# Performance work log

Hardware: AMD Instinct MI355X
Metric: run time of the kernel (lower is better)

The kernel has to match this reference:

```python
import jax, jax.numpy as jnp
import numpy as np

N_NODES = 100000
N_EDGES = 3200000
N_FEAT = 128
EMBED = 20
N_CLASSES = 10
N_GRAPHS = 64


def setup_inputs() -> dict:
    key = jax.random.key(0)
    ks = jax.random.split(key, 8)
    x = jax.random.normal(ks[0], (N_NODES, N_FEAT), dtype=jnp.float32)
    edge_index = jax.random.randint(ks[1], (2, N_EDGES), 0, N_NODES, dtype=jnp.int64)
    edge_weights = jax.random.uniform(ks[2], (N_EDGES,), dtype=jnp.float32)
    batch = jnp.sort(jax.random.randint(ks[3], (N_NODES,), 0, N_GRAPHS, dtype=jnp.int64))
    # GCNConv parameters (glorot-ish scale) and final linear layer
    W = jax.random.normal(ks[4], (N_FEAT, EMBED), dtype=jnp.float32) * (1.0 / np.sqrt(N_FEAT))
    b = jnp.zeros((EMBED,), dtype=jnp.float32)
    lin_W = jax.random.normal(ks[5], (2 * EMBED, N_CLASSES), dtype=jnp.float32) * (1.0 / np.sqrt(2 * EMBED))
    lin_b = jnp.zeros((N_CLASSES,), dtype=jnp.float32)
    return {"x": x, "edge_index": edge_index, "edge_weights": edge_weights,
            "batch": batch, "W": W, "b": b, "lin_W": lin_W, "lin_b": lin_b}


def reference(x, edge_index, edge_weights, batch, W, b, lin_W, lin_b):
    N = x.shape[0]
    # --- GCNConv with self-loops and symmetric normalization (PyG semantics) ---
    loops = jnp.arange(N, dtype=edge_index.dtype)
    src = jnp.concatenate([edge_index[0], loops])
    dst = jnp.concatenate([edge_index[1], loops])
    w = jnp.concatenate([edge_weights, jnp.ones((N,), dtype=edge_weights.dtype)])
    deg = jax.ops.segment_sum(w, dst, num_segments=N)  # degree at targets
    dinv = jnp.where(deg > 0, jax.lax.rsqrt(deg), 0.0)
    norm = dinv[src] * w * dinv[dst]  # [E+N]
    xw = x @ W  # [N, EMBED]
    msg = xw[src] * norm[:, None]  # gather + scale
    out1 = jax.ops.segment_sum(msg, dst, num_segments=N) + b  # scatter-add
    # --- L2 normalize per node (F.normalize p=2 dim=1, eps=1e-12), then ReLU ---
    nrm = jnp.sqrt(jnp.sum(out1 * out1, axis=1, keepdims=True))
    embed = jax.nn.relu(out1 / jnp.maximum(nrm, 1e-12))
    # --- global max / mean pool per graph ---
    mx = jax.ops.segment_max(embed, batch, num_segments=N_GRAPHS)
    mx = jnp.where(jnp.isfinite(mx), mx, 0.0)  # empty graphs -> 0
    cnt = jax.ops.segment_sum(jnp.ones((N,), dtype=embed.dtype), batch, num_segments=N_GRAPHS)
    mean = jax.ops.segment_sum(embed, batch, num_segments=N_GRAPHS) / jnp.maximum(cnt, 1.0)[:, None]
    pooled = jnp.concatenate([mx, mean], axis=-1)  # [G, 2*EMBED]
    return pooled @ lin_W + lin_b
```

## Files before the change

kernel.cpp:

```cpp
#include <hip/hip_runtime.h>
#include <hip/hip_fp16.h>

#define NN 100000
#define NE 3200000
#define NF 128
#define EM 20
#define NC 10
#define NG 64

#define NB 782
#define CAPB 4608
#define T 4096
#define SBLK 1024
#define NXW 391
#define GSPAN 16

__global__ __launch_bounds__(SBLK) void k_scatfat(
        const int* __restrict__ src, const int* __restrict__ dst,
        const float* __restrict__ w, int* __restrict__ gcursor,
        uint2* __restrict__ barr,
        const float* __restrict__ x, const float* __restrict__ W,
        float* __restrict__ xwf) {
    __shared__ __align__(16) char smem[52352];
    int tid = threadIdx.x;

    if (blockIdx.x < NXW) {
        float* Ws = (float*)smem;
        for (int i = tid; i < NF * EM; i += SBLK) Ws[i] = W[i];
        __syncthreads();
        int node = blockIdx.x * 256 + (tid >> 2);
        int j0 = (tid & 3) * 5;
        if (node >= NN) return;
        float acc[5] = {0.f, 0.f, 0.f, 0.f, 0.f};
        const float4* xr = (const float4*)(x + (size_t)node * NF);
        for (int k4 = 0; k4 < NF / 4; ++k4) {
            float4 xc = xr[k4];
            const float* wr = Ws + (k4 * 4) * EM + j0;
#pragma unroll
            for (int jj = 0; jj < 5; ++jj) acc[jj] = fmaf(xc.x, wr[jj], acc[jj]);
            wr += EM;
#pragma unroll
            for (int jj = 0; jj < 5; ++jj) acc[jj] = fmaf(xc.y, wr[jj], acc[jj]);
            wr += EM;
#pragma unroll
            for (int jj = 0; jj < 5; ++jj) acc[jj] = fmaf(xc.z, wr[jj], acc[jj]);
            wr += EM;
#pragma unroll
            for (int jj = 0; jj < 5; ++jj) acc[jj] = fmaf(xc.w, wr[jj], acc[jj]);
        }
        float* o = xwf + (size_t)node * EM + j0;
#pragma unroll
        for (int jj = 0; jj < 5; ++jj) o[jj] = acc[jj];
        return;
    }

    unsigned int* cnt   = (unsigned int*)smem;
    unsigned int* off   = (unsigned int*)(smem + 4096);
    unsigned int* gbase = (unsigned int*)(smem + 8192);
    unsigned int* wsum  = (unsigned int*)(smem + 11320);
    uint2*        staged= (uint2*)(smem + 11384);
    unsigned short* bkt = (unsigned short*)(smem + 44152);

    long E0 = (long)(blockIdx.x - NXW) * T;
    int tot = (int)min((long)T, (long)NE - E0);
    cnt[tid] = 0;
    __syncthreads();
    unsigned int dreg[T / SBLK];
#pragma unroll
    for (int k = 0; k < T / SBLK; ++k) {
        int e = k * SBLK + tid;
        dreg[k] = 0;
        if (e < tot) {
            dreg[k] = (unsigned)dst[E0 + e];
            atomicAdd(&cnt[dreg[k] >> 7], 1u);
        }
    }
    __syncthreads();
    {
        int lane = tid & 63, wv = tid >> 6;
        unsigned int v = cnt[tid];
        unsigned int s = v;
#pragma unroll
        for (int o = 1; o < 64; o <<= 1) {
            unsigned int t = __shfl_up(s, o);
            if (lane >= o) s += t;
        }
        if (lane == 63) wsum[wv] = s;
        __syncthreads();
        if (tid == 0) {
            unsigned int a = 0;
#pragma unroll
            for (int i = 0; i < 16; ++i) { unsigned int t = wsum[i]; wsum[i] = a; a += t; }
        }
        __syncthreads();
        off[tid] = wsum[wv] + s - v;
    }
    __syncthreads();
    if (tid < NB) {
        unsigned int c = cnt[tid];
        gbase[tid] = c ? (unsigned int)atomicAdd(&gcursor[tid], (int)c) : 0u;
        cnt[tid] = 0;
    }
    __syncthreads();
#pragma unroll
    for (int k = 0; k < T / SBLK; ++k) {
        int e = k * SBLK + tid;
        if (e < tot) {
            long ge = E0 + e;
            unsigned int d = dreg[k];
            unsigned int b = d >> 7;
            unsigned int slot = atomicAdd(&cnt[b], 1u);
            unsigned int pos = off[b] + slot;
            staged[pos] = make_uint2((((unsigned)src[ge]) << 7) | (d & 127u),
                                     __float_as_uint(w[ge]));
            bkt[pos] = (unsigned short)b;
        }
    }
    __syncthreads();
    for (int i = tid; i < tot; i += SBLK) {
        unsigned int b = bkt[i];
        unsigned int gpos = gbase[b] + ((unsigned)i - off[b]);
        if (gpos < CAPB) barr[(size_t)b * CAPB + gpos] = staged[i];
    }
}

__global__ __launch_bounds__(1024) void k_degps(
        const int* __restrict__ gcursor, const uint2* __restrict__ barr,
        const float* __restrict__ xwf, float* __restrict__ dinv,
        __half* __restrict__ xwhA, __half* __restrict__ xwhB) {
    __shared__ float dacc[128];
    __shared__ float dvs[128];
    int bk = blockIdx.x, tid = threadIdx.x;
    if (tid < 128) dacc[tid] = 0.f;
    __syncthreads();
    int cntb = min(gcursor[bk], CAPB);
    const uint2* row = barr + (size_t)bk * CAPB;
    for (int i = tid; i < cntb; i += 1024) {
        uint2 r = row[i];
        atomicAdd(&dacc[r.x & 127u], __uint_as_float(r.y));
    }
    __syncthreads();
    if (tid < 128) {
        float dv = rsqrtf(1.0f + dacc[tid]);
        dvs[tid] = dv;
        int gd = bk * 128 + tid;
        if (gd < NN) dinv[gd] = dv;
    }
    __syncthreads();
    for (int i = tid; i < 128 * EM; i += 1024) {
        int n = i / EM, dim = i - n * EM;
        int gd = bk * 128 + n;
        if (gd < NN) {
            __half hv = __float2half(xwf[(size_t)gd * EM + dim] * dvs[n]);
            if (dim < 16) xwhA[(size_t)gd * 16 + dim] = hv;
            else          xwhB[(size_t)gd * 4 + (dim - 16)] = hv;
        }
    }
}

__device__ inline void unpack16(uint4 a0, uint4 a1, float* f) {
    const __half2* h = (const __half2*)&a0;
#pragma unroll
    for (int c = 0; c < 4; ++c) { float2 t = __half22float2(h[c]); f[2*c] = t.x; f[2*c+1] = t.y; }
    h = (const __half2*)&a1;
#pragma unroll
    for (int c = 0; c < 4; ++c) { float2 t = __half22float2(h[c]); f[8+2*c] = t.x; f[9+2*c] = t.y; }
}
__device__ inline void unpack4(uint2 b0, float* f) {
    const __half2* h = (const __half2*)&b0;
#pragma unroll
    for (int c = 0; c < 2; ++c) { float2 t = __half22float2(h[c]); f[2*c] = t.x; f[2*c+1] = t.y; }
}

__global__ void k_sortaggr(const int* __restrict__ gcursor,
                           const unsigned long long* __restrict__ barr64,
                           const __half* __restrict__ xwhA, const __half* __restrict__ xwhB,
                           const float* __restrict__ dinv, const float* __restrict__ b,
                           const int* __restrict__ batch,
                           float* __restrict__ gsum, int* __restrict__ gmaxI,
                           int* __restrict__ gcnt) {
    __shared__ unsigned long long srt[CAPB];
    __shared__ unsigned int cnt[128];
    __shared__ unsigned int off[128];
    __shared__ unsigned int wtot;
    __shared__ float lsum[GSPAN][EM];
    __shared__ int   lmaxI[GSPAN][EM];
    __shared__ int   lcnt[GSPAN];
    __shared__ int   gmin_s;
    int bk = blockIdx.x, tid = threadIdx.x;
    if (tid < 128) cnt[tid] = 0;
    for (int i = tid; i < GSPAN * EM; i += 512) { lsum[i / EM][i % EM] = 0.f; lmaxI[i / EM][i % EM] = 0; }
    if (tid < GSPAN) lcnt[tid] = 0;
    if (tid == 0) gmin_s = batch[bk * 128];
    __syncthreads();
    int cntb = min(gcursor[bk], CAPB);
    const unsigned long long* row = barr64 + (size_t)bk * CAPB;
    unsigned long long rec[9];
    unsigned int pos[9];
    int K = 0;
    for (int e = tid; e < cntb; e += 512) {
        rec[K] = row[e];
        pos[K] = atomicAdd(&cnt[(unsigned)rec[K] & 127u], 1u);
        ++K;
    }
    __syncthreads();
    unsigned int v = 0, s = 0;
    if (tid < 128) {
        v = cnt[tid]; s = v;
#pragma unroll
        for (int o = 1; o < 64; o <<= 1) {
            unsigned int t = __shfl_up(s, o);
            if ((tid & 63) >= o) s += t;
        }
        if (tid == 63) wtot = s;
    }
    __syncthreads();
    if (tid < 128) {
        if (tid >= 64) s += wtot;
        off[tid] = s;
    }
    __syncthreads();
    for (int k = 0; k < K; ++k) {
        unsigned int dl = (unsigned)rec[k] & 127u;
        srt[off[dl] - cnt[dl] + pos[k]] = rec[k];
    }
    __syncthreads();
    int d = tid >> 2, sub = tid & 3;
    int s0 = (int)(off[d] - cnt[d]), s1 = (int)off[d];
    const uint4* pA = (const uint4*)xwhA;
    const uint2* pB = (const uint2*)xwhB;
    float acc[20];
#pragma unroll
    for (int j = 0; j < 20; ++j) acc[j] = 0.f;
    for (int e = s0 + sub; e < s1; e += 4) {
        unsigned long long r = srt[e];
        unsigned int sN = ((unsigned int)r) >> 7;
        float nw = __uint_as_float((unsigned int)(r >> 32));
        uint4 a0 = pA[(size_t)sN * 2];
        uint4 a1 = pA[(size_t)sN * 2 + 1];
        uint2 b0 = pB[sN];
        float f[20];
        unpack16(a0, a1, f);
        unpack4(b0, f + 16);
#pragma unroll
        for (int j = 0; j < 20; ++j) acc[j] = fmaf(f[j], nw, acc[j]);
    }
#pragma unroll
    for (int j = 0; j < 20; ++j) {
        acc[j] += __shfl_xor(acc[j], 1);
        acc[j] += __shfl_xor(acc[j], 2);
    }
    if (sub == 0) {
        int gd = bk * 128 + d;
        if (gd < NN) {
            float dv = dinv[gd];
            uint4 a0 = pA[(size_t)gd * 2];
            uint4 a1 = pA[(size_t)gd * 2 + 1];
            uint2 b0 = pB[gd];
            float xdh[20];
            unpack16(a0, a1, xdh);
            unpack4(b0, xdh + 16);
            float r[20];
            float ss = 0.f;
#pragma unroll
            for (int j = 0; j < 20; ++j) {
                r[j] = dv * (acc[j] + xdh[j]) + b[j];
                ss = fmaf(r[j], r[j], ss);
            }
            float inv = 1.0f / fmaxf(sqrtf(ss), 1e-12f);
            float o[20];
#pragma unroll
            for (int j = 0; j < 20; ++j) {
                float e2 = r[j] * inv;
                o[j] = e2 > 0.f ? e2 : 0.f;
            }
            int g = batch[gd];
            int gl = g - gmin_s;
            if (gl < GSPAN) {
#pragma unroll
                for (int j = 0; j < 20; ++j) {
                    atomicAdd(&lsum[gl][j], o[j]);
                    atomicMax(&lmaxI[gl][j], __float_as_int(o[j]));
                }
                atomicAdd(&lcnt[gl], 1);
            } else {
#pragma unroll
                for (int j = 0; j < 20; ++j) {
                    atomicAdd(&gsum[g * EM + j], o[j]);
                    atomicMax(&gmaxI[g * EM + j], __float_as_int(o[j]));
                }
                atomicAdd(&gcnt[g], 1);
            }
        }
    }
    __syncthreads();
    for (int i = tid; i < GSPAN * EM; i += 512) {
        int gl = i / EM, j = i - gl * EM;
        int g = gmin_s + gl;
        if (g < NG && lcnt[gl] > 0) {
            atomicAdd(&gsum[g * EM + j], lsum[gl][j]);
            atomicMax(&gmaxI[g * EM + j], lmaxI[gl][j]);
        }
    }
    if (tid < GSPAN) {
        int g = gmin_s + tid;
        if (g < NG && lcnt[tid] > 0) atomicAdd(&gcnt[g], lcnt[tid]);
    }
}

__global__ void k_final(const float* __restrict__ gsum, const int* __restrict__ gmaxI,
                        const int* __restrict__ gcnt,
                        const float* __restrict__ lw, const float* __restrict__ lb,
                        float* __restrict__ out) {
    __shared__ float pooled[2 * EM];
    int g = blockIdx.x, tid = threadIdx.x;
    if (tid < EM) pooled[tid] = __int_as_float(gmaxI[g * EM + tid]);
    else if (tid < 2 * EM) {
        float c = (float)gcnt[g];
        pooled[tid] = gsum[g * EM + (tid - EM)] / fmaxf(c, 1.0f);
    }
    __syncthreads();
    if (tid < NC) {
        float acc = lb[tid];
#pragma unroll
        for (int j = 0; j < 2 * EM; ++j) acc = fmaf(pooled[j], lw[j * NC + tid], acc);
        out[g * NC + tid] = acc;
    }
}

static inline size_t align_up(size_t v) { return (v + 1023) & ~(size_t)1023; }

extern "C" void kernel_launch(void* const* d_in, const int* in_sizes, int n_in,
                              void* d_out, int out_size, void* d_ws, size_t ws_size,
                              hipStream_t stream) {
    const float* x     = (const float*)d_in[0];
    const int*   ei    = (const int*)d_in[1];
    const float* ew    = (const float*)d_in[2];
    const int*   batch = (const int*)d_in[3];
    const float* W     = (const float*)d_in[4];
    const float* b     = (const float*)d_in[5];
    const float* lw    = (const float*)d_in[6];
    const float* lb    = (const float*)d_in[7];
    float* out = (float*)d_out;

    char* ws = (char*)d_ws;
    int*    gcursor = (int*)ws;    ws += align_up(4096);
    char*   poolws  = ws;          ws += align_up(5120 + 5120 + 256);
    float*  gsum    = (float*)poolws;
    int*    gmaxI   = (int*)(poolws + 5120);
    int*    gcnt    = (int*)(poolws + 10240);
    float*  dinv    = (float*)ws;  ws += align_up((size_t)NN * 4);
    __half* xwhA    = (__half*)ws; ws += align_up((size_t)NN * 16 * 2);
    __half* xwhB    = (__half*)ws; ws += align_up((size_t)NN * 4 * 2);
    float*  xwf     = (float*)ws;  ws += align_up((size_t)NN * EM * 4);
    uint2*  barr    = (uint2*)ws;
    unsigned long long* barr64 = (unsigned long long*)barr;

    const int* srcp = ei;
    const int* dstp = ei + NE;

    (void)hipMemsetAsync(gcursor, 0, align_up(4096) + align_up(10496), stream);
    k_scatfat<<<NXW + (NE + T - 1) / T, SBLK, 0, stream>>>(srcp, dstp, ew, gcursor, barr,
                                                           x, W, xwf);
    k_degps<<<NB, 1024, 0, stream>>>(gcursor, barr, xwf, dinv, xwhA, xwhB);
    k_sortaggr<<<NB, 512, 0, stream>>>(gcursor, barr64, xwhA, xwhB, dinv, b,
                                       batch, gsum, gmaxI, gcnt);
    k_final<<<NG, 64, 0, stream>>>(gsum, gmaxI, gcnt, lw, lb, out);
}
```

Before: 232.4 us.

## Fuse final linear into aggregation via last-block pattern and spread pooling atomics

Drops the separate k_final launch: each k_sortaggr block bumps a completion counter, and the last block to finish reads the pooled sums, max and counts and computes the output linear layer. The per-node pooling atomics are also spread across the four sub-lanes (5 features each) instead of being issued serially by lane 0. This removes one kernel launch and shortens the serial atomic tail per node. In exchange every block pays a device-scope atomic and an extra barrier, and the final linear now runs on a single block.

```diff
diff --git a/kernel.cpp b/kernel.cpp
--- a/kernel.cpp
+++ b/kernel.cpp
@@ -178,7 +178,9 @@
                            const float* __restrict__ dinv, const float* __restrict__ b,
                            const int* __restrict__ batch,
                            float* __restrict__ gsum, int* __restrict__ gmaxI,
-                           int* __restrict__ gcnt) {
+                           int* __restrict__ gcnt, int* donecnt,
+                           const float* __restrict__ lw, const float* __restrict__ lb,
+                           float* __restrict__ out) {
     __shared__ unsigned long long srt[CAPB];
     __shared__ unsigned int cnt[128];
     __shared__ unsigned int off[128];
@@ -187,6 +189,7 @@
     __shared__ int   lmaxI[GSPAN][EM];
     __shared__ int   lcnt[GSPAN];
     __shared__ int   gmin_s;
+    __shared__ int   isLast;
     int bk = blockIdx.x, tid = threadIdx.x;
     if (tid < 128) cnt[tid] = 0;
     for (int i = tid; i < GSPAN * EM; i += 512) { lsum[i / EM][i % EM] = 0.f; lmaxI[i / EM][i % EM] = 0; }
@@ -250,47 +253,43 @@
         acc[j] += __shfl_xor(acc[j], 1);
         acc[j] += __shfl_xor(acc[j], 2);
     }
-    if (sub == 0) {
-        int gd = bk * 128 + d;
-        if (gd < NN) {
-            float dv = dinv[gd];
-            uint4 a0 = pA[(size_t)gd * 2];
-            uint4 a1 = pA[(size_t)gd * 2 + 1];
-            uint2 b0 = pB[gd];
-            float xdh[20];
-            unpack16(a0, a1, xdh);
-            unpack4(b0, xdh + 16);
-            float r[20];
-            float ss = 0.f;
-#pragma unroll
-            for (int j = 0; j < 20; ++j) {
-                r[j] = dv * (acc[j] + xdh[j]) + b[j];
-                ss = fmaf(r[j], r[j], ss);
+    int gd = bk * 128 + d;
+    if (gd < NN) {
+        float dv = dinv[gd];
+        uint4 a0 = pA[(size_t)gd * 2];
+        uint4 a1 = pA[(size_t)gd * 2 + 1];
+        uint2 b0 = pB[gd];
+        float xdh[20];
+        unpack16(a0, a1, xdh);
+        unpack4(b0, xdh + 16);
+        float r[20];
+        float ss = 0.f;
+#pragma unroll
+        for (int j = 0; j < 20; ++j) {
+            r[j] = dv * (acc[j] + xdh[j]) + b[j];
+            ss = fmaf(r[j], r[j], ss);
+        }
+        float inv = 1.0f / fmaxf(sqrtf(ss), 1e-12f);
+        int g = batch[gd];
+        int gl = g - gmin_s;
+        bool inT = gl < GSPAN;
+#pragma unroll
+        for (int j = 0; j < 20; ++j) {
+            float e2 = r[j] * inv;
+            float oj = e2 > 0.f ? e2 : 0.f;
+            if (sub == j / 5) {
+                if (inT) {
+                    atomicAdd(&lsum[gl][j], oj);
+                    atomicMax(&lmaxI[gl][j], __float_as_int(oj));
+                } else {
+                    atomicAdd(&gsum[g * EM + j], oj);
+                    atomicMax(&gmaxI[g * EM + j], __float_as_int(oj));
+                }
             }
-            float inv = 1.0f / fmaxf(sqrtf(ss), 1e-12f);
-            float o[20];
-#pragma unroll
-            for (int j = 0; j < 20; ++j) {
-                float e2 = r[j] * inv;
-                o[j] = e2 > 0.f ? e2 : 0.f;
-            }
-            int g = batch[gd];
-            int gl = g - gmin_s;
-            if (gl < GSPAN) {
-#pragma unroll
-                for (int j = 0; j < 20; ++j) {
-                    atomicAdd(&lsum[gl][j], o[j]);
-                    atomicMax(&lmaxI[gl][j], __float_as_int(o[j]));
-                }
-                atomicAdd(&lcnt[gl], 1);
-            } else {
-#pragma unroll
-                for (int j = 0; j < 20; ++j) {
-                    atomicAdd(&gsum[g * EM + j], o[j]);
-                    atomicMax(&gmaxI[g * EM + j], __float_as_int(o[j]));
-                }
-                atomicAdd(&gcnt[g], 1);
-            }
+        }
+        if (sub == 0) {
+            if (inT) atomicAdd(&lcnt[gl], 1);
+            else     atomicAdd(&gcnt[g], 1);
         }
     }
     __syncthreads();
@@ -306,25 +305,31 @@
         int g = gmin_s + tid;
         if (g < NG && lcnt[tid] > 0) atomicAdd(&gcnt[g], lcnt[tid]);
     }
-}
-
-__global__ void k_final(const float* __restrict__ gsum, const int* __restrict__ gmaxI,
-                        const int* __restrict__ gcnt,
-                        const float* __restrict__ lw, const float* __restrict__ lb,
-                        float* __restrict__ out) {
-    __shared__ float pooled[2 * EM];
-    int g = blockIdx.x, tid = threadIdx.x;
-    if (tid < EM) pooled[tid] = __int_as_float(gmaxI[g * EM + tid]);
-    else if (tid < 2 * EM) {
-        float c = (float)gcnt[g];
-        pooled[tid] = gsum[g * EM + (tid - EM)] / fmaxf(c, 1.0f);
-    }
-    __syncthreads();
-    if (tid < NC) {
-        float acc = lb[tid];
-#pragma unroll
-        for (int j = 0; j < 2 * EM; ++j) acc = fmaf(pooled[j], lw[j * NC + tid], acc);
-        out[g * NC + tid] = acc;
+    __syncthreads();
+    if (tid == 0) {
+        int done = __hip_atomic_fetch_add(donecnt, 1, __ATOMIC_ACQ_REL,
+                                          __HIP_MEMORY_SCOPE_AGENT);
+        isLast = (done == NB - 1);
+    }
+    __syncthreads();
+    if (isLast) {
+        float (*pld)[2 * EM] = (float(*)[2 * EM])srt;
+        for (int i = tid; i < NG * EM; i += 512) {
+            int g = i / EM, j = i - g * EM;
+            int mi = __hip_atomic_load(&gmaxI[i], __ATOMIC_RELAXED, __HIP_MEMORY_SCOPE_AGENT);
+            float sm = __hip_atomic_load(&gsum[i], __ATOMIC_RELAXED, __HIP_MEMORY_SCOPE_AGENT);
+            int c = __hip_atomic_load(&gcnt[g], __ATOMIC_RELAXED, __HIP_MEMORY_SCOPE_AGENT);
+            pld[g][j] = __int_as_float(mi);
+            pld[g][EM + j] = sm / fmaxf((float)c, 1.0f);
+        }
+        __syncthreads();
+        for (int i = tid; i < NG * NC; i += 512) {
+            int g = i / NC, c = i - g * NC;
+            float acc2 = lb[c];
+#pragma unroll
+            for (int j = 0; j < 2 * EM; ++j) acc2 = fmaf(pld[g][j], lw[j * NC + c], acc2);
+            out[g * NC + c] = acc2;
+        }
     }
 }
 
@@ -345,10 +350,11 @@
 
     char* ws = (char*)d_ws;
     int*    gcursor = (int*)ws;    ws += align_up(4096);
-    char*   poolws  = ws;          ws += align_up(5120 + 5120 + 256);
+    char*   poolws  = ws;          ws += align_up(12288);
     float*  gsum    = (float*)poolws;
     int*    gmaxI   = (int*)(poolws + 5120);
     int*    gcnt    = (int*)(poolws + 10240);
+    int*    donecnt = (int*)(poolws + 10496);
     float*  dinv    = (float*)ws;  ws += align_up((size_t)NN * 4);
     __half* xwhA    = (__half*)ws; ws += align_up((size_t)NN * 16 * 2);
     __half* xwhB    = (__half*)ws; ws += align_up((size_t)NN * 4 * 2);
@@ -359,11 +365,10 @@
     const int* srcp = ei;
     const int* dstp = ei + NE;
 
-    (void)hipMemsetAsync(gcursor, 0, align_up(4096) + align_up(10496), stream);
+    (void)hipMemsetAsync(gcursor, 0, align_up(4096) + align_up(12288), stream);
     k_scatfat<<<NXW + (NE + T - 1) / T, SBLK, 0, stream>>>(srcp, dstp, ew, gcursor, barr,
                                                            x, W, xwf);
     k_degps<<<NB, 1024, 0, stream>>>(gcursor, barr, xwf, dinv, xwhA, xwhB);
     k_sortaggr<<<NB, 512, 0, stream>>>(gcursor, barr64, xwhA, xwhB, dinv, b,
-                                       batch, gsum, gmaxI, gcnt);
-    k_final<<<NG, 64, 0, stream>>>(gsum, gmaxI, gcnt, lw, lb, out);
-}
+                                       batch, gsum, gmaxI, gcnt, donecnt, lw, lb, out);
+}
```

Result: slower. 244.0 us (+5.0%).
